# Performance work log

Measured on AMD Instinct MI355X. Metric: run time of the kernel, lower is better.

## Reference

```python
import jax, jax.numpy as jnp
import numpy as np

B, N, E, C_IN, C_OUT = 16, 4096, 131072, 256, 256


def setup_inputs() -> dict:
    key = jax.random.key(0)
    k1, k2, k3, k4 = jax.random.split(key, 4)
    x = jax.random.normal(k1, (B, N, C_IN), dtype=jnp.float32)
    edge_index = jax.random.randint(k2, (B, 2, E), 0, N, dtype=jnp.int32)
    edge_weight = jax.random.uniform(k3, (B, E), dtype=jnp.float32)
    # glorot init for weight [C_in, C_out]
    scale = float(np.sqrt(6.0 / (C_IN + C_OUT)))
    W = jax.random.uniform(k4, (C_IN, C_OUT), dtype=jnp.float32, minval=-scale, maxval=scale)
    return {"x": x, "edge_index": edge_index, "edge_weight": edge_weight, "W": W}


def _gcn_one_graph(xi, ei, ewi, W):
    # xi: [N, C_in], ei: [2, E+N], ewi: [E+N]
    n = xi.shape[0]
    row, col = ei[0], ei[1]
    deg = jax.ops.segment_sum(ewi, row, num_segments=n)            # [N]
    deg_inv = jnp.where(deg > 0, jax.lax.rsqrt(deg), 0.0)          # deg^-0.5, inf -> 0
    norm = deg_inv[row] * ewi * deg_inv[col]                       # [E+N]
    xw = xi @ W                                                    # [N, C_out]
    msg = norm[:, None] * xw[col]                                  # gather + scale
    out = jax.ops.segment_sum(msg, row, num_segments=n)            # scatter-add to rows
    return jax.nn.relu(out)                                        # act = F.relu, bias=False


def reference(x, edge_index, edge_weight, W):
    b, n, _ = x.shape
    # add self loops with weight 1 (fill_value=1)
    loop = jnp.arange(n, dtype=edge_index.dtype)
    loop_idx = jnp.broadcast_to(jnp.stack([loop, loop])[None], (b, 2, n))
    ei = jnp.concatenate([edge_index, loop_idx], axis=-1)          # [B, 2, E+N]
    ew = jnp.concatenate([edge_weight, jnp.ones((b, n), x.dtype)], axis=-1)  # [B, E+N]
    return jax.vmap(_gcn_one_graph, in_axes=(0, 0, 0, None))(x, ei, ew, W)
```

## Files before the change

### kernel.cpp

```cpp
#include <hip/hip_runtime.h>
#include <cstdint>
#include <cstddef>

#define BB 16
#define NN 4096
#define EE 131072
#define CIN 256
#define COUT 256
#define NCH 16
#define CHE (EE / NCH)

typedef __attribute__((ext_vector_type(8))) _Float16 h16x8;
typedef __attribute__((ext_vector_type(4))) float f32x4;

__global__ __launch_bounds__(256) void phaseA_kernel(const float* __restrict__ W, _Float16* __restrict__ wt,
                                                     const int* __restrict__ ei, const float* __restrict__ ew,
                                                     int* __restrict__ chist, float* __restrict__ wdeg) {
    __shared__ int h[NN];
    __shared__ float wh[NN];
    int bid = blockIdx.x;
    int tid = threadIdx.x;
    if (bid < BB * NCH) {
        int b = bid >> 4, c = bid & (NCH - 1);
        for (int i = tid; i < NN; i += 256) { h[i] = 0; wh[i] = 0.f; }
        __syncthreads();
        const int* rows = ei + (size_t)b * 2 * EE + (size_t)c * CHE;
        const float* w = ew + (size_t)b * EE + (size_t)c * CHE;
        #pragma unroll 4
        for (int j = 0; j < CHE / 256; ++j) {
            int row = rows[j * 256 + tid];
            float wv = w[j * 256 + tid];
            atomicAdd(&h[row], 1);
            atomicAdd(&wh[row], wv);
        }
        __syncthreads();
        int* co = chist + ((size_t)b * NCH + c) * NN;
        float* wo = wdeg + ((size_t)b * NCH + c) * NN;
        for (int i = tid; i < NN; i += 256) { co[i] = h[i]; wo[i] = wh[i]; }
    } else {
        int n = bid - BB * NCH;
        int k = tid;
        wt[n * CIN + k] = (_Float16)W[(size_t)k * COUT + n];
    }
}

__global__ __launch_bounds__(1024) void scanfused_kernel(const int* __restrict__ chist, const float* __restrict__ wdeg,
                                                         int* __restrict__ chunkbase, int* __restrict__ roff,
                                                         float* __restrict__ dinv) {
    int b = blockIdx.x, tid = threadIdx.x;
    int wid = tid >> 6, lane = tid & 63;
    __shared__ int wsum[16];
    __shared__ int wbase[16];
    __shared__ int gtot_s;
    int carry = 0;
    for (int g = 0; g < 4; ++g) {
        int r = g * 1024 + tid;
        int cv[NCH];
        int tot = 0;
        float dsum = 1.0f;
        #pragma unroll
        for (int c = 0; c < NCH; ++c) {
            size_t idx = ((size_t)b * NCH + c) * NN + r;
            cv[c] = chist[idx];
            tot += cv[c];
            dsum += wdeg[idx];
        }
        dinv[b * NN + r] = rsqrtf(dsum);
        int incl = tot;
        #pragma unroll
        for (int off = 1; off < 64; off <<= 1) {
            int t = __shfl_up(incl, off, 64);
            if (lane >= off) incl += t;
        }
        if (lane == 63) wsum[wid] = incl;
        __syncthreads();
        if (wid == 0) {
            int v = (lane < 16) ? wsum[lane] : 0;
            int winc = v;
            #pragma unroll
            for (int off = 1; off < 16; off <<= 1) {
                int t = __shfl_up(winc, off, 64);
                if (lane >= off) winc += t;
            }
            if (lane < 16) wbase[lane] = winc - v;
            if (lane == 15) gtot_s = winc;
        }
        __syncthreads();
        int excl = carry + wbase[wid] + (incl - tot);
        roff[b * NN + r] = excl;
        int acc = excl;
        #pragma unroll
        for (int c = 0; c < NCH; ++c) {
            chunkbase[((size_t)b * NCH + c) * NN + r] = acc;
            acc += cv[c];
        }
        carry += gtot_s;
        __syncthreads();
    }
}

__global__ __launch_bounds__(256) void scatter2_kernel(const int* __restrict__ ei, const float* __restrict__ ew,
                                                       const float* __restrict__ dinv, const int* __restrict__ chunkbase,
                                                       uint32_t* __restrict__ csr) {
    __shared__ int basebuf[NN];
    __shared__ float dinvs[NN];
    int bid = blockIdx.x;
    int xcd = bid & 7;
    int j = bid >> 3;
    int b = xcd * 2 + (j >> 4);
    int c = j & (NCH - 1);
    int tid = threadIdx.x;
    for (int i = tid; i < NN; i += 256) {
        basebuf[i] = chunkbase[((size_t)b * NCH + c) * NN + i];
        dinvs[i] = dinv[b * NN + i];
    }
    __syncthreads();
    const int* rows = ei + (size_t)b * 2 * EE + (size_t)c * CHE;
    const int* cols = rows + EE;
    const float* w = ew + (size_t)b * EE + (size_t)c * CHE;
    uint32_t* cs = csr + (size_t)b * EE;
    #pragma unroll 4
    for (int jj = 0; jj < CHE / 256; ++jj) {
        int e = jj * 256 + tid;
        int row = rows[e];
        int col = cols[e];
        float nm = dinvs[row] * w[e] * dinvs[col];
        int pos = atomicAdd(&basebuf[row], 1);
        uint32_t nmh = (uint32_t)__builtin_bit_cast(unsigned short, (_Float16)nm);
        cs[pos] = ((uint32_t)col << 16) | nmh;
    }
}

__global__ __launch_bounds__(256) void gemm_f32src_kernel(const float* __restrict__ x, const _Float16* __restrict__ wt,
                                                          _Float16* __restrict__ xw) {
    __shared__ _Float16 As[128][64];
    __shared__ _Float16 Bs[128][64];
    int tid = threadIdx.x;
    int lane = tid & 63;
    int wave = tid >> 6;
    int row0 = blockIdx.x * 128;
    int col0 = blockIdx.y * 128;
    int wr = wave >> 1, wc = wave & 1;
    int hi = lane >> 4, lo = lane & 15;
    f32x4 acc[4][4] = {};
    for (int kk = 0; kk < CIN; kk += 64) {
        #pragma unroll
        for (int j = 0; j < 4; ++j) {
            int c = j * 256 + tid;
            int r = c >> 3, kq = c & 7;
            const float* g = &x[(size_t)(row0 + r) * CIN + kk + 8 * kq];
            float4 f0 = *reinterpret_cast<const float4*>(g);
            float4 f1 = *reinterpret_cast<const float4*>(g + 4);
            h16x8 v;
            v[0] = (_Float16)f0.x; v[1] = (_Float16)f0.y; v[2] = (_Float16)f0.z; v[3] = (_Float16)f0.w;
            v[4] = (_Float16)f1.x; v[5] = (_Float16)f1.y; v[6] = (_Float16)f1.z; v[7] = (_Float16)f1.w;
            *reinterpret_cast<h16x8*>(&As[r][8 * kq]) = v;
        }
        #pragma unroll
        for (int j = 0; j < 4; ++j) {
            int c = j * 256 + tid;
            int r = c >> 3, kq = c & 7;
            *reinterpret_cast<h16x8*>(&Bs[r][8 * kq]) =
                *reinterpret_cast<const h16x8*>(&wt[(size_t)(col0 + r) * CIN + kk + 8 * kq]);
        }
        __syncthreads();
        #pragma unroll
        for (int ks = 0; ks < 2; ++ks) {
            h16x8 a[4], b[4];
            #pragma unroll
            for (int m = 0; m < 4; ++m)
                a[m] = *reinterpret_cast<const h16x8*>(&As[wr * 64 + m * 16 + lo][ks * 32 + 8 * hi]);
            #pragma unroll
            for (int n = 0; n < 4; ++n)
                b[n] = *reinterpret_cast<const h16x8*>(&Bs[wc * 64 + n * 16 + lo][ks * 32 + 8 * hi]);
            #pragma unroll
            for (int m = 0; m < 4; ++m)
                #pragma unroll
                for (int n = 0; n < 4; ++n)
                    acc[m][n] = __builtin_amdgcn_mfma_f32_16x16x32_f16(a[m], b[n], acc[m][n], 0, 0, 0);
        }
        __syncthreads();
    }
    #pragma unroll
    for (int m = 0; m < 4; ++m)
        #pragma unroll
        for (int n = 0; n < 4; ++n)
            #pragma unroll
            for (int r = 0; r < 4; ++r) {
                int row = row0 + wr * 64 + m * 16 + hi * 4 + r;
                int col = col0 + wc * 64 + n * 16 + lo;
                xw[(size_t)row * COUT + col] = (_Float16)acc[m][n][r];
            }
}

#define MIXQLO(acc_, w_, qv_) asm("v_fma_mix_f32 %0, %1, %2, %0 op_sel:[0,0,0] op_sel_hi:[1,1,0]" \
                                  : "+v"(acc_) : "v"(w_), "v"(qv_));
#define MIXQHI(acc_, w_, qv_) asm("v_fma_mix_f32 %0, %1, %2, %0 op_sel:[1,0,0] op_sel_hi:[1,1,0]" \
                                  : "+v"(acc_) : "v"(w_), "v"(qv_));
#define ACCMIXQ(w_, qv_) { \
    MIXQLO(a0, (w_).x, qv_); MIXQHI(a1, (w_).x, qv_); \
    MIXQLO(a2, (w_).y, qv_); MIXQHI(a3, (w_).y, qv_); \
    MIXQLO(a4, (w_).z, qv_); MIXQHI(a5, (w_).z, qv_); \
    MIXQLO(a6, (w_).w, qv_); MIXQHI(a7, (w_).w, qv_); }
#define MIXSLO(acc_, w_, nm_) asm("v_fma_mix_f32 %0, %1, %2, %0 op_sel:[0,0,0] op_sel_hi:[1,0,0]" \
                                  : "+v"(acc_) : "v"(w_), "v"(nm_));
#define MIXSHI(acc_, w_, nm_) asm("v_fma_mix_f32 %0, %1, %2, %0 op_sel:[1,0,0] op_sel_hi:[1,0,0]" \
                                  : "+v"(acc_) : "v"(w_), "v"(nm_));

__global__ __launch_bounds__(256) void aggregate_kernel(const _Float16* __restrict__ xw, const float* __restrict__ dinv,
                                                        const int* __restrict__ roff, const uint32_t* __restrict__ csr,
                                                        float* __restrict__ out) {
    int bid = blockIdx.x;
    int xcd = bid & 7;
    int idx = bid >> 3;
    int b = xcd * 2 + (idx >> 10);
    int rowblk = idx & 1023;
    int wave = threadIdx.x >> 6;
    int lane = threadIdx.x & 63;
    int n = rowblk * 4 + wave;
    bool hiHalf = lane >= 32;
    int sub = lane & 31;
    uint32_t lanebyte = sub * 16;

    const int* rb = roff + b * NN;
    int s = __builtin_amdgcn_readfirstlane(rb[n]);
    int eRaw = (n == NN - 1) ? EE : rb[n + 1];
    int e = __builtin_amdgcn_readfirstlane(eRaw);
    int cnt = e - s;
    const uint32_t* cs = csr + (size_t)b * EE + s;

    const char* xwbase = (const char*)(xw + (size_t)b * NN * COUT);
    float a0 = 0.f, a1 = 0.f, a2 = 0.f, a3 = 0.f, a4 = 0.f, a5 = 0.f, a6 = 0.f, a7 = 0.f;

    {
        float di = dinv[b * NN + n];
        float sn = hiHalf ? 0.f : di * di;
        uint4 w = *reinterpret_cast<const uint4*>(xwbase + (size_t)n * (COUT * 2) + lanebyte);
        MIXSLO(a0, w.x, sn); MIXSHI(a1, w.x, sn);
        MIXSLO(a2, w.y, sn); MIXSHI(a3, w.y, sn);
        MIXSLO(a4, w.z, sn); MIXSHI(a5, w.z, sn);
        MIXSLO(a6, w.w, sn); MIXSHI(a7, w.w, sn);
    }

    int m = cnt & ~7;
    int i = 0;
    for (; i < m; i += 8) {
        uint32_t q[8];
        #pragma unroll
        for (int u = 0; u < 8; ++u) q[u] = cs[i + u];
        #pragma unroll
        for (int u = 0; u < 4; ++u) {
            uint32_t qv = hiHalf ? q[2 * u + 1] : q[2 * u];
            uint32_t offx = ((qv >> 16) << 9) + lanebyte;
            uint4 w = *reinterpret_cast<const uint4*>(xwbase + offx);
            ACCMIXQ(w, qv);
        }
    }
    if (i < cnt) {
        #pragma unroll
        for (int u = 0; u < 4; ++u) {
            int j0 = i + 2 * u, j1 = j0 + 1;
            uint32_t q0 = cs[(j0 < cnt) ? j0 : cnt - 1];
            uint32_t q1 = cs[(j1 < cnt) ? j1 : cnt - 1];
            if (j0 >= cnt) q0 &= 0xFFFF0000u;
            if (j1 >= cnt) q1 &= 0xFFFF0000u;
            uint32_t qv = hiHalf ? q1 : q0;
            uint32_t offx = ((qv >> 16) << 9) + lanebyte;
            uint4 w = *reinterpret_cast<const uint4*>(xwbase + offx);
            ACCMIXQ(w, qv);
        }
    }

    a0 += __shfl(a0, lane ^ 32, 64); a1 += __shfl(a1, lane ^ 32, 64);
    a2 += __shfl(a2, lane ^ 32, 64); a3 += __shfl(a3, lane ^ 32, 64);
    a4 += __shfl(a4, lane ^ 32, 64); a5 += __shfl(a5, lane ^ 32, 64);
    a6 += __shfl(a6, lane ^ 32, 64); a7 += __shfl(a7, lane ^ 32, 64);

    float4 o = hiHalf
        ? make_float4(fmaxf(a4, 0.f), fmaxf(a5, 0.f), fmaxf(a6, 0.f), fmaxf(a7, 0.f))
        : make_float4(fmaxf(a0, 0.f), fmaxf(a1, 0.f), fmaxf(a2, 0.f), fmaxf(a3, 0.f));
    float* orow = out + ((size_t)b * NN + n) * COUT + sub * 8 + (hiHalf ? 4 : 0);
    *reinterpret_cast<float4*>(orow) = o;
}

__global__ __launch_bounds__(256) void cvt_wt_kernel(const float* __restrict__ W, _Float16* __restrict__ wt) {
    int n = blockIdx.x;
    int k = threadIdx.x;
    wt[n * CIN + k] = (_Float16)W[(size_t)k * COUT + n];
}

__global__ __launch_bounds__(256) void init_deg_kernel(float* __restrict__ deg, float v) {
    int i = blockIdx.x * 256 + threadIdx.x;
    if (i < BB * NN) deg[i] = v;
}

__global__ __launch_bounds__(256) void deg_only_kernel(const int* __restrict__ ei, const float* __restrict__ ew,
                                                       float* __restrict__ deg) {
    int idx = blockIdx.x * 256 + threadIdx.x;
    if (idx >= BB * EE) return;
    int b = idx / EE, e = idx - b * EE;
    atomicAdd(&deg[b * NN + ei[(size_t)b * 2 * EE + e]], ew[(size_t)b * EE + e]);
}

__global__ __launch_bounds__(256) void deginv_kernel(const float* __restrict__ deg, float* __restrict__ dinv) {
    int i = blockIdx.x * 256 + threadIdx.x;
    if (i < BB * NN) {
        float d = deg[i];
        dinv[i] = (d > 0.0f) ? rsqrtf(d) : 0.0f;
    }
}

__global__ __launch_bounds__(256) void self_kernel(const _Float16* __restrict__ xw, const float* __restrict__ dinv,
                                                   float* __restrict__ out) {
    int bn = blockIdx.x;
    int c = threadIdx.x;
    float di = dinv[bn];
    out[(size_t)bn * COUT + c] = di * di * (float)xw[(size_t)bn * COUT + c];
}

__global__ __launch_bounds__(256) void scatter_atomic_kernel(const int* __restrict__ ei, const float* __restrict__ ew,
                                                             const float* __restrict__ dinv,
                                                             const _Float16* __restrict__ xw, float* __restrict__ out) {
    int be = blockIdx.x;
    int b = be / EE, e = be - b * EE;
    int c = threadIdx.x;
    int row = ei[(size_t)b * 2 * EE + e];
    int col = ei[(size_t)b * 2 * EE + EE + e];
    float w = ew[(size_t)b * EE + e];
    float nm = dinv[b * NN + row] * w * dinv[b * NN + col];
    const _Float16* xwb = xw + (size_t)b * NN * COUT;
    atomicAdd(&out[((size_t)b * NN + row) * COUT + c], nm * (float)xwb[(size_t)col * COUT + c]);
}

__global__ __launch_bounds__(256) void relu_kernel(float* __restrict__ out) {
    size_t i = (size_t)blockIdx.x * 256 + threadIdx.x;
    out[i] = fmaxf(out[i], 0.0f);
}

extern "C" void kernel_launch(void* const* d_in, const int* in_sizes, int n_in,
                              void* d_out, int out_size, void* d_ws, size_t ws_size,
                              hipStream_t stream) {
    const float* x  = (const float*)d_in[0];
    const int*   ei = (const int*)d_in[1];
    const float* ew = (const float*)d_in[2];
    const float* Wm = (const float*)d_in[3];
    float* out = (float*)d_out;

    char* ws = (char*)d_ws;
    size_t off = 0;
    auto alloc = [&](size_t bytes) -> void* {
        void* p = ws + off;
        off += (bytes + 255) & ~(size_t)255;
        return p;
    };
    _Float16* xw        = (_Float16*)alloc((size_t)BB * NN * COUT * 2);
    int*      chist     = (int*)alloc((size_t)BB * NCH * NN * 4);
    float*    wdeg      = (float*)alloc((size_t)BB * NCH * NN * 4);
    int*      chunkbase = (int*)alloc((size_t)BB * NCH * NN * 4);
    int*      roff      = (int*)alloc((size_t)BB * NN * 4);
    float*    dinv      = (float*)alloc((size_t)BB * NN * 4);
    _Float16* wt        = (_Float16*)alloc((size_t)CIN * COUT * 2);
    uint32_t* csr       = (uint32_t*)chist;
    float*    deg_fb    = (float*)chist;
    bool use_csr = (ws_size >= off);

    if (use_csr) {
        phaseA_kernel<<<BB * NCH + COUT, 256, 0, stream>>>(Wm, wt, ei, ew, chist, wdeg);
        scanfused_kernel<<<BB, 1024, 0, stream>>>(chist, wdeg, chunkbase, roff, dinv);
        scatter2_kernel<<<BB * NCH, 256, 0, stream>>>(ei, ew, dinv, chunkbase, csr);
        dim3 ggrid((BB * NN) / 128, COUT / 128);
        gemm_f32src_kernel<<<ggrid, 256, 0, stream>>>(x, wt, xw);
        aggregate_kernel<<<BB * NN / 4, 256, 0, stream>>>(xw, dinv, roff, csr, out);
    } else {
        const int bnBlocks = (BB * NN) / 256;
        cvt_wt_kernel<<<COUT, CIN, 0, stream>>>(Wm, wt);
        init_deg_kernel<<<bnBlocks, 256, 0, stream>>>(deg_fb, 1.0f);
        deg_only_kernel<<<(BB * EE) / 256, 256, 0, stream>>>(ei, ew, deg_fb);
        deginv_kernel<<<bnBlocks, 256, 0, stream>>>(deg_fb, dinv);
        dim3 ggrid((BB * NN) / 128, COUT / 128);
        gemm_f32src_kernel<<<ggrid, 256, 0, stream>>>(x, wt, xw);
        self_kernel<<<BB * NN, 256, 0, stream>>>(xw, dinv, out);
        scatter_atomic_kernel<<<BB * EE, 256, 0, stream>>>(ei, ew, dinv, xw, out);
        relu_kernel<<<(BB * NN * COUT) / 256, 256, 0, stream>>>(out);
    }
}
```

Measured before the change: 133.4 us.

## Widen GEMM tile to full output width and swizzle LDS layout

The GEMM now uses 512-thread blocks that compute a 128x256 output tile, covering the full COUT, instead of 128x128 tiles in a 2D grid. Each row of x is therefore read and converted from fp32 once instead of twice. LDS accesses use an XOR swizzle on 16-byte chunks to avoid bank conflicts on the strided fragment reads. The trade-off is more LDS per block (48KB allocated) and fewer, larger blocks, which may lower occupancy.

```diff
diff --git a/kernel.cpp b/kernel.cpp
--- a/kernel.cpp
+++ b/kernel.cpp
@@ -131,22 +131,24 @@
     }
 }
 
-__global__ __launch_bounds__(256) void gemm_f32src_kernel(const float* __restrict__ x, const _Float16* __restrict__ wt,
-                                                          _Float16* __restrict__ xw) {
-    __shared__ _Float16 As[128][64];
-    __shared__ _Float16 Bs[128][64];
+#define SWZ(byte_, row_) ((byte_) ^ (((row_) & 7) << 4))
+__global__ __launch_bounds__(512) void gemm_wide_kernel(const float* __restrict__ x, const _Float16* __restrict__ wt,
+                                                        _Float16* __restrict__ xw) {
+    __shared__ __align__(16) char smem[49152];
+    char* As = smem;
+    char* Bs = smem + 16384;
     int tid = threadIdx.x;
     int lane = tid & 63;
-    int wave = tid >> 6;
+    int wid = tid >> 6;
+    int wr = wid >> 2, wc = wid & 3;
+    int hi = lane >> 4, lo = lane & 15;
     int row0 = blockIdx.x * 128;
-    int col0 = blockIdx.y * 128;
-    int wr = wave >> 1, wc = wave & 1;
-    int hi = lane >> 4, lo = lane & 15;
     f32x4 acc[4][4] = {};
+
     for (int kk = 0; kk < CIN; kk += 64) {
         #pragma unroll
-        for (int j = 0; j < 4; ++j) {
-            int c = j * 256 + tid;
+        for (int j = 0; j < 2; ++j) {
+            int c = j * 512 + tid;
             int r = c >> 3, kq = c & 7;
             const float* g = &x[(size_t)(row0 + r) * CIN + kk + 8 * kq];
             float4 f0 = *reinterpret_cast<const float4*>(g);
@@ -154,25 +156,29 @@
             h16x8 v;
             v[0] = (_Float16)f0.x; v[1] = (_Float16)f0.y; v[2] = (_Float16)f0.z; v[3] = (_Float16)f0.w;
             v[4] = (_Float16)f1.x; v[5] = (_Float16)f1.y; v[6] = (_Float16)f1.z; v[7] = (_Float16)f1.w;
-            *reinterpret_cast<h16x8*>(&As[r][8 * kq]) = v;
+            *reinterpret_cast<h16x8*>(As + SWZ(r * 128 + kq * 16, r)) = v;
         }
         #pragma unroll
         for (int j = 0; j < 4; ++j) {
-            int c = j * 256 + tid;
+            int c = j * 512 + tid;
             int r = c >> 3, kq = c & 7;
-            *reinterpret_cast<h16x8*>(&Bs[r][8 * kq]) =
-                *reinterpret_cast<const h16x8*>(&wt[(size_t)(col0 + r) * CIN + kk + 8 * kq]);
+            *reinterpret_cast<h16x8*>(Bs + SWZ(r * 128 + kq * 16, r)) =
+                *reinterpret_cast<const h16x8*>(&wt[(size_t)r * CIN + kk + 8 * kq]);
         }
         __syncthreads();
         #pragma unroll
         for (int ks = 0; ks < 2; ++ks) {
             h16x8 a[4], b[4];
             #pragma unroll
-            for (int m = 0; m < 4; ++m)
-                a[m] = *reinterpret_cast<const h16x8*>(&As[wr * 64 + m * 16 + lo][ks * 32 + 8 * hi]);
-            #pragma unroll
-            for (int n = 0; n < 4; ++n)
-                b[n] = *reinterpret_cast<const h16x8*>(&Bs[wc * 64 + n * 16 + lo][ks * 32 + 8 * hi]);
+            for (int m = 0; m < 4; ++m) {
+                int r = wr * 64 + m * 16 + lo;
+                a[m] = *reinterpret_cast<const h16x8*>(As + SWZ(r * 128 + ks * 64 + hi * 16, r));
+            }
+            #pragma unroll
+            for (int n = 0; n < 4; ++n) {
+                int r = wc * 64 + n * 16 + lo;
+                b[n] = *reinterpret_cast<const h16x8*>(Bs + SWZ(r * 128 + ks * 64 + hi * 16, r));
+            }
             #pragma unroll
             for (int m = 0; m < 4; ++m)
                 #pragma unroll
@@ -188,7 +194,7 @@
             #pragma unroll
             for (int r = 0; r < 4; ++r) {
                 int row = row0 + wr * 64 + m * 16 + hi * 4 + r;
-                int col = col0 + wc * 64 + n * 16 + lo;
+                int col = wc * 64 + n * 16 + lo;
                 xw[(size_t)row * COUT + col] = (_Float16)acc[m][n][r];
             }
 }
@@ -368,8 +374,7 @@
         phaseA_kernel<<<BB * NCH + COUT, 256, 0, stream>>>(Wm, wt, ei, ew, chist, wdeg);
         scanfused_kernel<<<BB, 1024, 0, stream>>>(chist, wdeg, chunkbase, roff, dinv);
         scatter2_kernel<<<BB * NCH, 256, 0, stream>>>(ei, ew, dinv, chunkbase, csr);
-        dim3 ggrid((BB * NN) / 128, COUT / 128);
-        gemm_f32src_kernel<<<ggrid, 256, 0, stream>>>(x, wt, xw);
+        gemm_wide_kernel<<<BB * NN / 128, 512, 0, stream>>>(x, wt, xw);
         aggregate_kernel<<<BB * NN / 4, 256, 0, stream>>>(xw, dinv, roff, csr, out);
     } else {
         const int bnBlocks = (BB * NN) / 256;
@@ -377,8 +382,7 @@
         init_deg_kernel<<<bnBlocks, 256, 0, stream>>>(deg_fb, 1.0f);
         deg_only_kernel<<<(BB * EE) / 256, 256, 0, stream>>>(ei, ew, deg_fb);
         deginv_kernel<<<bnBlocks, 256, 0, stream>>>(deg_fb, dinv);
-        dim3 ggrid((BB * NN) / 128, COUT / 128);
-        gemm_f32src_kernel<<<ggrid, 256, 0, stream>>>(x, wt, xw);
+        gemm_wide_kernel<<<BB * NN / 128, 512, 0, stream>>>(x, wt, xw);
         self_kernel<<<BB * NN, 256, 0, stream>>>(xw, dinv, out);
         scatter_atomic_kernel<<<BB * EE, 256, 0, stream>>>(ei, ew, dinv, xw, out);
         relu_kernel<<<(BB * NN * COUT) / 256, 256, 0, stream>>>(out);
```

New measurement: 123.1 us. -7.7%, faster.
